# Kernel optimization log

Hardware: AMD Instinct MI355X
Metric: run time of the kernel (lower is better)

Reference implementation:

```python
import jax, jax.numpy as jnp
import numpy as np

CTX = 2048
N_EMBD = 1024
HEAD = 128

def setup_inputs() -> dict:
    key = jax.random.key(0)
    kx, kq, kk, kv = jax.random.split(key, 4)
    s = 1.0 / np.sqrt(N_EMBD)
    return {
        "x": jax.random.normal(kx, (4, CTX, N_EMBD), dtype=jnp.float32),
        "Wq": jax.random.normal(kq, (N_EMBD, HEAD), dtype=jnp.float32) * s,
        "Wk": jax.random.normal(kk, (N_EMBD, HEAD), dtype=jnp.float32) * s,
        "Wv": jax.random.normal(kv, (N_EMBD, HEAD), dtype=jnp.float32) * s,
    }

def reference(x, Wq, Wk, Wv):
    B, T, C = x.shape
    q = jnp.einsum('btc,ch->bth', x, Wq)
    k = jnp.einsum('btc,ch->bth', x, Wk)
    v = jnp.einsum('btc,ch->bth', x, Wv)
    scale = 1.0 / jnp.sqrt(jnp.asarray(k.shape[-1], dtype=x.dtype))
    wei = jnp.einsum('bth,bsh->bts', q, k) * scale  # [B,T,T]
    causal = jnp.tril(jnp.ones((T, T), dtype=bool))
    wei = jnp.where(causal, wei, jnp.asarray(-jnp.inf, dtype=wei.dtype))
    wei = jax.nn.softmax(wei, axis=-1)
    out = jnp.einsum('bts,bsh->bth', wei, v)
    return out
```

## Files before the change

### kernel.cpp

```cpp
#include <hip/hip_runtime.h>

#define BATCH 4
#define CTX   2048
#define EMB   1024
#define HEAD  128

typedef __attribute__((ext_vector_type(8))) short bf16x8;
typedef __attribute__((ext_vector_type(4))) float f32x4;
typedef const __attribute__((address_space(1))) unsigned int* gas_t;
typedef __attribute__((address_space(3))) unsigned int* las_t;

#define FINF (__builtin_inff())
__device__ inline float fexp2(float x) { return __builtin_amdgcn_exp2f(x); }

__device__ inline void cp16(const void* g, void* l) {
    __builtin_amdgcn_global_load_lds((gas_t)g, (las_t)l, 16, 0, 0);
}

__device__ inline unsigned short f2bf(float f) {
    union { float f; unsigned u; } v; v.f = f;
    unsigned r = v.u + 0x7fffu + ((v.u >> 16) & 1u);
    return (unsigned short)(r >> 16);
}
__device__ inline unsigned pk2(float a, float b) {
    return (unsigned)f2bf(a) | ((unsigned)f2bf(b) << 16);
}

__global__ __launch_bounds__(256)
void transpose_w_kernel(const float* __restrict__ Wq, const float* __restrict__ Wk,
                        const float* __restrict__ Wv, unsigned short* __restrict__ Wt) {
    const int k0 = blockIdx.x * 64;
    const int h0 = blockIdx.y * 64;
    const int w  = blockIdx.z;
    const float* W = (w == 0) ? Wq : (w == 1) ? Wk : Wv;
    __shared__ float Ts[64][65];
    const int tid = threadIdx.x;
    #pragma unroll
    for (int it = 0; it < 4; ++it) {
        const int kk = (tid >> 4) + it * 16;
        const int c4 = (tid & 15) * 4;
        const float4 f = *(const float4*)&W[(size_t)(k0 + kk) * HEAD + h0 + c4];
        Ts[kk][c4 + 0] = f.x; Ts[kk][c4 + 1] = f.y;
        Ts[kk][c4 + 2] = f.z; Ts[kk][c4 + 3] = f.w;
    }
    __syncthreads();
    const int hr  = tid >> 2;
    const int kc0 = (tid & 3) * 16;
    union { unsigned short s[16]; uint4 q[2]; } tmp;
    #pragma unroll
    for (int i = 0; i < 16; ++i) tmp.s[i] = f2bf(Ts[kc0 + i][hr]);
    unsigned short* dst = &Wt[(size_t)w * HEAD * EMB + (size_t)(h0 + hr) * EMB + k0 + kc0];
    ((uint4*)dst)[0] = tmp.q[0];
    ((uint4*)dst)[1] = tmp.q[1];
}

__global__ __launch_bounds__(128, 3)
void proj_kernel(const float* __restrict__ x, const unsigned short* __restrict__ Wt,
                 unsigned short* __restrict__ qb, unsigned short* __restrict__ kb,
                 unsigned short* __restrict__ vt) {
    __shared__ __align__(16) char smem[24576];
    char* Ab = smem;
    char* Bb = smem + 8192;

    const int wsel = blockIdx.y;
    const int tid  = threadIdx.x;
    const int wv   = tid >> 6;
    const int lane = tid & 63;
    const int p = lane >> 4, c = lane & 15;
    const int m0 = blockIdx.x * 32;
    const unsigned short* Wp = Wt + (size_t)wsel * HEAD * EMB;

    const int u7  = c & 7;
    const int u2c = (c ^ (c >> 2)) & 3;

    auto stage = [&](int bi, int ks) {
        #pragma unroll
        for (int i = 0; i < 2; ++i) {
            const int f = i * 128 + tid;
            const int r = f >> 3, s = f & 7, q = s ^ (r & 7);
            cp16(&x[(size_t)(m0 + r) * EMB + ks * 32 + q * 4],
                 Ab + bi * 4096 + i * 2048 + wv * 1024);
        }
        #pragma unroll
        for (int i = 0; i < 4; ++i) {
            const int f = i * 128 + tid;
            const int h = f >> 2, s = f & 3, q = s ^ ((h ^ (h >> 2)) & 3);
            cp16(&Wp[(size_t)h * EMB + ks * 32 + q * 8],
                 Bb + bi * 8192 + i * 2048 + wv * 1024);
        }
    };

    auto xfrag = [&](const char* Ac, int r) {
        const float4 a0 = *(const float4*)(Ac + r * 128 + (((2 * p)     ^ u7) * 16));
        const float4 a1 = *(const float4*)(Ac + r * 128 + (((2 * p + 1) ^ u7) * 16));
        union { unsigned u[4]; bf16x8 v; } xf;
        xf.u[0] = pk2(a0.x, a0.y); xf.u[1] = pk2(a0.z, a0.w);
        xf.u[2] = pk2(a1.x, a1.y); xf.u[3] = pk2(a1.z, a1.w);
        return xf.v;
    };

    if (wsel < 2) {
        f32x4 acc[8];
        #pragma unroll
        for (int i = 0; i < 8; ++i) acc[i] = (f32x4){0.f, 0.f, 0.f, 0.f};
        stage(0, 0);
        for (int ks = 0; ks < 32; ++ks) {
            const int cur = ks & 1;
            __syncthreads();
            if (ks + 1 < 32) stage(cur ^ 1, ks + 1);
            const bf16x8 xv = xfrag(Ab + cur * 4096, wv * 16 + c);
            const char* Bc = Bb + cur * 8192;
            #pragma unroll
            for (int nt = 0; nt < 8; ++nt) {
                const int h = nt * 16 + c;
                const bf16x8 wf = *(const bf16x8*)(Bc + h * 64 + ((p ^ u2c) * 16));
                acc[nt] = __builtin_amdgcn_mfma_f32_16x16x32_bf16(xv, wf, acc[nt], 0, 0, 0);
            }
        }
        unsigned short* outp = (wsel == 0) ? qb : kb;
        #pragma unroll
        for (int rr = 0; rr < 4; ++rr) {
            unsigned short* orow = outp + (size_t)(m0 + wv * 16 + p * 4 + rr) * HEAD + c;
            #pragma unroll
            for (int nt = 0; nt < 8; ++nt)
                orow[nt * 16] = f2bf(acc[nt][rr]);
        }
    } else {
        f32x4 acc[4][2];
        #pragma unroll
        for (int i = 0; i < 4; ++i)
            #pragma unroll
            for (int j = 0; j < 2; ++j) acc[i][j] = (f32x4){0.f, 0.f, 0.f, 0.f};
        stage(0, 0);
        for (int ks = 0; ks < 32; ++ks) {
            const int cur = ks & 1;
            __syncthreads();
            if (ks + 1 < 32) stage(cur ^ 1, ks + 1);
            const char* Ac = Ab + cur * 4096;
            const char* Bc = Bb + cur * 8192;
            bf16x8 xv[2];
            #pragma unroll
            for (int n2 = 0; n2 < 2; ++n2) xv[n2] = xfrag(Ac, n2 * 16 + c);
            #pragma unroll
            for (int mt = 0; mt < 4; ++mt) {
                const int h = wv * 64 + mt * 16 + c;
                const bf16x8 wf = *(const bf16x8*)(Bc + h * 64 + ((p ^ u2c) * 16));
                #pragma unroll
                for (int n2 = 0; n2 < 2; ++n2)
                    acc[mt][n2] = __builtin_amdgcn_mfma_f32_16x16x32_bf16(wf, xv[n2], acc[mt][n2], 0, 0, 0);
            }
        }
        const int bidx = m0 >> 11;
        const int tl   = m0 & (CTX - 1);
        unsigned short* vbp = vt + (size_t)bidx * HEAD * CTX;
        #pragma unroll
        for (int mt = 0; mt < 4; ++mt)
            #pragma unroll
            for (int rr = 0; rr < 4; ++rr) {
                const int h = wv * 64 + mt * 16 + p * 4 + rr;
                #pragma unroll
                for (int n2 = 0; n2 < 2; ++n2)
                    vbp[(size_t)h * CTX + tl + n2 * 16 + c] = f2bf(acc[mt][n2][rr]);
            }
    }
}

__global__ __launch_bounds__(64, 1)
void attn_kernel(const unsigned short* __restrict__ qb,
                 const unsigned short* __restrict__ kb,
                 const unsigned short* __restrict__ vt,
                 float* __restrict__ out) {
    __shared__ __align__(16) char smem[65536];
    char* Kb = smem;
    char* Vb = smem + 32768;

    const int bx   = blockIdx.x;
    const int b    = bx & 3;
    const int tile = 127 - (bx >> 2);
    const int lane = threadIdx.x;
    const int p = lane >> 4, c = lane & 15;
    const int t0 = tile * 16;
    const int qg = t0 + c;
    const int u7 = c & 7;

    const unsigned short* kbat = kb + (size_t)b * CTX * HEAD;
    const unsigned short* vbat = vt + (size_t)b * HEAD * CTX;

    bf16x8 qf[4];
    #pragma unroll
    for (int ks = 0; ks < 4; ++ks)
        qf[ks] = *(const bf16x8*)&qb[((size_t)b * CTX + t0 + c) * HEAD + ks * 32 + p * 8];

    f32x4 o[8];
    #pragma unroll
    for (int i = 0; i < 8; ++i) o[i] = (f32x4){0.f, 0.f, 0.f, 0.f};
    float m = -FINF, l = 0.f;

    const int  slA = 32 * (p & 1) + c;
    const int  slB = slA + 16;
    const bool thi = (p >> 1) != 0;
    const int  nsteps = (tile + 4) >> 2;
    const float scale2 = 0.08838834764831845f * 1.44269504088896340f;

    auto stage = [&](int bi, int js) {
        const unsigned short* kg = kbat + (size_t)(js * 64) * HEAD;
        #pragma unroll
        for (int i = 0; i < 16; ++i) {
            const int f = i * 64 + lane;
            const int r = f >> 4, s = f & 15, q = s ^ (r & 7);
            cp16(kg + (size_t)r * HEAD + q * 8, Kb + bi * 16384 + i * 1024);
        }
        #pragma unroll
        for (int i = 0; i < 16; ++i) {
            const int f = i * 64 + lane;
            const int r = f >> 3, s = f & 7, q = s ^ (r & 7);
            cp16(vbat + (size_t)r * CTX + js * 64 + q * 8, Vb + bi * 16384 + i * 1024);
        }
    };

    stage(0, 0);
    for (int js = 0; js < nsteps; ++js) {
        const int cur = js & 1;
        __builtin_amdgcn_s_waitcnt(0);

        bf16x8 kfr[4][4], vfr[2][8];
        #pragma unroll
        for (int nt = 0; nt < 4; ++nt) {
            const char* rp = Kb + cur * 16384 + (nt * 16 + c) * 256;
            #pragma unroll
            for (int ks = 0; ks < 4; ++ks)
                kfr[nt][ks] = *(const bf16x8*)(rp + (((ks * 4 + p) ^ u7) * 16));
        }
        #pragma unroll
        for (int mt = 0; mt < 8; ++mt) {
            const char* rp = Vb + cur * 16384 + (mt * 16 + c) * 128;
            #pragma unroll
            for (int ch = 0; ch < 2; ++ch)
                vfr[ch][mt] = *(const bf16x8*)(rp + (((ch * 4 + p) ^ u7) * 16));
        }

        if (js + 1 < nsteps) stage(cur ^ 1, js + 1);

        const int c0 = js * 64;
        f32x4 st[4];
        #pragma unroll
        for (int nt = 0; nt < 4; ++nt) st[nt] = (f32x4){0.f, 0.f, 0.f, 0.f};
        #pragma unroll
        for (int ks = 0; ks < 4; ++ks)
            #pragma unroll
            for (int nt = 0; nt < 4; ++nt)
                st[nt] = __builtin_amdgcn_mfma_f32_16x16x32_bf16(kfr[nt][ks], qf[ks], st[nt], 0, 0, 0);

        float s[4][4];
        float lm = -FINF;
        if (js == nsteps - 1) {
            #pragma unroll
            for (int nt = 0; nt < 4; ++nt)
                #pragma unroll
                for (int r = 0; r < 4; ++r) {
                    const int kv = c0 + nt * 16 + p * 4 + r;
                    float v = st[nt][r] * scale2;
                    v = (kv <= qg) ? v : -FINF;
                    s[nt][r] = v;
                    lm = fmaxf(lm, v);
                }
        } else {
            #pragma unroll
            for (int nt = 0; nt < 4; ++nt)
                #pragma unroll
                for (int r = 0; r < 4; ++r) {
                    const float v = st[nt][r] * scale2;
                    s[nt][r] = v;
                    lm = fmaxf(lm, v);
                }
        }
        lm = fmaxf(lm, __shfl_xor(lm, 16, 64));
        lm = fmaxf(lm, __shfl_xor(lm, 32, 64));
        const float m_new = fmaxf(m, lm);
        const float alpha = fexp2(m - m_new);
        float ls = 0.f;
        #pragma unroll
        for (int nt = 0; nt < 4; ++nt)
            #pragma unroll
            for (int r = 0; r < 4; ++r) {
                const float pv = fexp2(s[nt][r] - m_new);
                s[nt][r] = pv;
                ls += pv;
            }
        ls += __shfl_xor(ls, 16, 64);
        ls += __shfl_xor(ls, 32, 64);
        l = l * alpha + ls;
        m = m_new;
        #pragma unroll
        for (int i = 0; i < 8; ++i) {
            o[i][0] *= alpha; o[i][1] *= alpha;
            o[i][2] *= alpha; o[i][3] *= alpha;
        }
        #pragma unroll
        for (int ch = 0; ch < 2; ++ch) {
            const unsigned pa0 = pk2(s[2*ch][0],     s[2*ch][1]);
            const unsigned pb0 = pk2(s[2*ch][2],     s[2*ch][3]);
            const unsigned pa1 = pk2(s[2*ch + 1][0], s[2*ch + 1][1]);
            const unsigned pb1 = pk2(s[2*ch + 1][2], s[2*ch + 1][3]);
            const unsigned u0a = __shfl((int)pa0, slA, 64), u0b = __shfl((int)pa1, slA, 64);
            const unsigned u1a = __shfl((int)pb0, slA, 64), u1b = __shfl((int)pb1, slA, 64);
            const unsigned u2a = __shfl((int)pa0, slB, 64), u2b = __shfl((int)pa1, slB, 64);
            const unsigned u3a = __shfl((int)pb0, slB, 64), u3b = __shfl((int)pb1, slB, 64);
            union { unsigned u[4]; bf16x8 v; } pf;
            pf.u[0] = thi ? u0b : u0a;
            pf.u[1] = thi ? u1b : u1a;
            pf.u[2] = thi ? u2b : u2a;
            pf.u[3] = thi ? u3b : u3a;
            #pragma unroll
            for (int mt = 0; mt < 8; ++mt)
                o[mt] = __builtin_amdgcn_mfma_f32_16x16x32_bf16(vfr[ch][mt], pf.v, o[mt], 0, 0, 0);
        }
    }

    const float linv = 1.f / l;
    float* orow = out + ((size_t)b * CTX + t0 + c) * HEAD;
    #pragma unroll
    for (int mt = 0; mt < 8; ++mt) {
        float4 ov = make_float4(o[mt][0] * linv, o[mt][1] * linv,
                                o[mt][2] * linv, o[mt][3] * linv);
        *(float4*)&orow[mt * 16 + p * 4] = ov;
    }
}

extern "C" void kernel_launch(void* const* d_in, const int* in_sizes, int n_in,
                              void* d_out, int out_size, void* d_ws, size_t ws_size,
                              hipStream_t stream) {
    const float* x  = (const float*)d_in[0];
    const float* Wq = (const float*)d_in[1];
    const float* Wk = (const float*)d_in[2];
    const float* Wv = (const float*)d_in[3];
    float* out = (float*)d_out;

    unsigned short* Wt = (unsigned short*)d_ws;
    unsigned short* qb = Wt + (size_t)3 * HEAD * EMB;
    unsigned short* kb = qb + (size_t)BATCH * CTX * HEAD;
    unsigned short* vt = kb + (size_t)BATCH * CTX * HEAD;

    transpose_w_kernel<<<dim3(16, 2, 3), 256, 0, stream>>>(Wq, Wk, Wv, Wt);
    proj_kernel<<<dim3((BATCH * CTX) / 32, 3), 128, 0, stream>>>(x, Wt, qb, kb, vt);
    attn_kernel<<<BATCH * (CTX / 16), 64, 0, stream>>>(qb, kb, vt, out);
}
```

Measured before the change: 146.0 us.

## Split causal attention into KV chunks with partial outputs and a merge kernel

Replaces the single-wave-per-16-row attention kernel with a split-KV scheme. Each 256-thread block handles 64 query rows, and the KV range is cut into 512-key chunks so that long causal rows are spread over several blocks. Partial outputs go to workspace as bf16 along with the running max and sum, and a second kernel merges them with softmax rescaling. This aims to improve load balance and share each K/V tile across four waves, at the cost of an extra launch, workspace traffic and bf16 rounding of the partial outputs. It falls back to the old kernel if the workspace is too small.

```diff
diff --git a/kernel.cpp b/kernel.cpp
--- a/kernel.cpp
+++ b/kernel.cpp
@@ -24,6 +24,9 @@
 }
 __device__ inline unsigned pk2(float a, float b) {
     return (unsigned)f2bf(a) | ((unsigned)f2bf(b) << 16);
+}
+__device__ inline float bf2f(unsigned u16) {
+    union { unsigned u; float f; } v; v.u = u16 << 16; return v.f;
 }
 
 __global__ __launch_bounds__(256)
@@ -89,7 +92,6 @@
                  Bb + bi * 8192 + i * 2048 + wv * 1024);
         }
     };
-
     auto xfrag = [&](const char* Ac, int r) {
         const float4 a0 = *(const float4*)(Ac + r * 128 + (((2 * p)     ^ u7) * 16));
         const float4 a1 = *(const float4*)(Ac + r * 128 + (((2 * p + 1) ^ u7) * 16));
@@ -165,6 +167,236 @@
     }
 }
 
+__global__ __launch_bounds__(256, 2)
+void attn_split_kernel(const unsigned short* __restrict__ qb,
+                       const unsigned short* __restrict__ kb,
+                       const unsigned short* __restrict__ vt,
+                       unsigned short* __restrict__ pO,
+                       float* __restrict__ pM, float* __restrict__ pL) {
+    __shared__ __align__(16) char smem[65536];
+    char* Kb = smem;
+    char* Vb = smem + 32768;
+
+    const int g = blockIdx.x;
+    const int b = blockIdx.y;
+    int T, ch;
+    if (g < 8)       { T = g;                ch = 0; }
+    else if (g < 24) { T = 8  + ((g - 8) >> 1);  ch = (g - 8) & 1; }
+    else if (g < 48) { T = 16 + (g - 24) / 3;    ch = (g - 24) % 3; }
+    else             { T = 24 + ((g - 48) >> 2); ch = (g - 48) & 3; }
+    const int nch    = (T >> 3) + 1;
+    const int kstart = ch * 512;
+    const int kend   = min(kstart + 512, 64 * (T + 1));
+    const int nsteps = (kend - kstart) >> 6;
+    const bool lastchunk = (ch == nch - 1);
+
+    const int tid  = threadIdx.x;
+    const int wv   = tid >> 6;
+    const int lane = tid & 63;
+    const int p = lane >> 4, c = lane & 15;
+    const int t0 = T * 64;
+    const int qg = t0 + wv * 16 + c;
+    const int u7 = c & 7;
+
+    const unsigned short* kbat = kb + (size_t)b * CTX * HEAD;
+    const unsigned short* vbat = vt + (size_t)b * HEAD * CTX;
+
+    bf16x8 qf[4];
+    #pragma unroll
+    for (int ks = 0; ks < 4; ++ks)
+        qf[ks] = *(const bf16x8*)&qb[((size_t)b * CTX + t0 + wv * 16 + c) * HEAD + ks * 32 + p * 8];
+
+    f32x4 o[8];
+    #pragma unroll
+    for (int i = 0; i < 8; ++i) o[i] = (f32x4){0.f, 0.f, 0.f, 0.f};
+    float m = -FINF, l = 0.f;
+
+    const int  slA = 32 * (p & 1) + c;
+    const int  slB = slA + 16;
+    const bool thi = (p >> 1) != 0;
+    const float scale2 = 0.08838834764831845f * 1.44269504088896340f;
+
+    auto stage = [&](int bi, int js) {
+        const unsigned short* kg = kbat + (size_t)(kstart + js * 64) * HEAD;
+        #pragma unroll
+        for (int i = 0; i < 4; ++i) {
+            const int f = i * 256 + tid;
+            const int r = f >> 4, s = f & 15, q = s ^ (r & 7);
+            cp16(kg + (size_t)r * HEAD + q * 8, Kb + bi * 16384 + (f >> 6) * 1024);
+        }
+        const unsigned short* vg = vbat + kstart + js * 64;
+        #pragma unroll
+        for (int i = 0; i < 4; ++i) {
+            const int f = i * 256 + tid;
+            const int r = f >> 3, s = f & 7, q = s ^ (r & 7);
+            cp16(vg + (size_t)r * CTX + q * 8, Vb + bi * 16384 + (f >> 6) * 1024);
+        }
+    };
+
+    stage(0, 0);
+    for (int js = 0; js < nsteps; ++js) {
+        const int cur = js & 1;
+        __builtin_amdgcn_s_waitcnt(0);
+        __syncthreads();
+
+        bf16x8 kfr[4][4];
+        #pragma unroll
+        for (int nt = 0; nt < 4; ++nt) {
+            const char* rp = Kb + cur * 16384 + (nt * 16 + c) * 256;
+            #pragma unroll
+            for (int ks = 0; ks < 4; ++ks)
+                kfr[nt][ks] = *(const bf16x8*)(rp + (((ks * 4 + p) ^ u7) * 16));
+        }
+        if (js + 1 < nsteps) stage(cur ^ 1, js + 1);
+
+        f32x4 st[4];
+        #pragma unroll
+        for (int nt = 0; nt < 4; ++nt) st[nt] = (f32x4){0.f, 0.f, 0.f, 0.f};
+        #pragma unroll
+        for (int ks = 0; ks < 4; ++ks)
+            #pragma unroll
+            for (int nt = 0; nt < 4; ++nt)
+                st[nt] = __builtin_amdgcn_mfma_f32_16x16x32_bf16(kfr[nt][ks], qf[ks], st[nt], 0, 0, 0);
+
+        bf16x8 vfr[2][8];
+        #pragma unroll
+        for (int mt = 0; mt < 8; ++mt) {
+            const char* rp = Vb + cur * 16384 + (mt * 16 + c) * 128;
+            #pragma unroll
+            for (int ch2 = 0; ch2 < 2; ++ch2)
+                vfr[ch2][mt] = *(const bf16x8*)(rp + (((ch2 * 4 + p) ^ u7) * 16));
+        }
+
+        float s[4][4];
+        float lm = -FINF;
+        if (lastchunk && js == nsteps - 1) {
+            #pragma unroll
+            for (int nt = 0; nt < 4; ++nt)
+                #pragma unroll
+                for (int r = 0; r < 4; ++r) {
+                    const int kv = kstart + js * 64 + nt * 16 + p * 4 + r;
+                    float v = st[nt][r] * scale2;
+                    v = (kv <= qg) ? v : -FINF;
+                    s[nt][r] = v;
+                    lm = fmaxf(lm, v);
+                }
+        } else {
+            #pragma unroll
+            for (int nt = 0; nt < 4; ++nt)
+                #pragma unroll
+                for (int r = 0; r < 4; ++r) {
+                    const float v = st[nt][r] * scale2;
+                    s[nt][r] = v;
+                    lm = fmaxf(lm, v);
+                }
+        }
+        lm = fmaxf(lm, __shfl_xor(lm, 16, 64));
+        lm = fmaxf(lm, __shfl_xor(lm, 32, 64));
+        const float m_new = fmaxf(m, lm);
+        const float alpha = fexp2(m - m_new);
+        float ls = 0.f;
+        #pragma unroll
+        for (int nt = 0; nt < 4; ++nt)
+            #pragma unroll
+            for (int r = 0; r < 4; ++r) {
+                const float pv = fexp2(s[nt][r] - m_new);
+                s[nt][r] = pv;
+                ls += pv;
+            }
+        ls += __shfl_xor(ls, 16, 64);
+        ls += __shfl_xor(ls, 32, 64);
+        l = l * alpha + ls;
+        m = m_new;
+        #pragma unroll
+        for (int i = 0; i < 8; ++i) {
+            o[i][0] *= alpha; o[i][1] *= alpha;
+            o[i][2] *= alpha; o[i][3] *= alpha;
+        }
+        #pragma unroll
+        for (int ch2 = 0; ch2 < 2; ++ch2) {
+            const unsigned pa0 = pk2(s[2*ch2][0],     s[2*ch2][1]);
+            const unsigned pb0 = pk2(s[2*ch2][2],     s[2*ch2][3]);
+            const unsigned pa1 = pk2(s[2*ch2 + 1][0], s[2*ch2 + 1][1]);
+            const unsigned pb1 = pk2(s[2*ch2 + 1][2], s[2*ch2 + 1][3]);
+            const unsigned u0a = __shfl((int)pa0, slA, 64), u0b = __shfl((int)pa1, slA, 64);
+            const unsigned u1a = __shfl((int)pb0, slA, 64), u1b = __shfl((int)pb1, slA, 64);
+            const unsigned u2a = __shfl((int)pa0, slB, 64), u2b = __shfl((int)pa1, slB, 64);
+            const unsigned u3a = __shfl((int)pb0, slB, 64), u3b = __shfl((int)pb1, slB, 64);
+            union { unsigned u[4]; bf16x8 v; } pf;
+            pf.u[0] = thi ? u0b : u0a;
+            pf.u[1] = thi ? u1b : u1a;
+            pf.u[2] = thi ? u2b : u2a;
+            pf.u[3] = thi ? u3b : u3a;
+            #pragma unroll
+            for (int mt = 0; mt < 8; ++mt)
+                o[mt] = __builtin_amdgcn_mfma_f32_16x16x32_bf16(vfr[ch2][mt], pf.v, o[mt], 0, 0, 0);
+        }
+    }
+
+    const size_t pbase = (size_t)(b * 32 + T) * 4 + ch;
+    unsigned short* po = pO + pbase * (64 * 128) + (wv * 16 + c) * 128;
+    #pragma unroll
+    for (int mt = 0; mt < 8; ++mt) {
+        union { unsigned short sh[4]; uint2 u; } t;
+        #pragma unroll
+        for (int r = 0; r < 4; ++r) t.sh[r] = f2bf(o[mt][r]);
+        *(uint2*)&po[mt * 16 + p * 4] = t.u;
+    }
+    if (p == 0) {
+        pM[pbase * 64 + wv * 16 + c] = m;
+        pL[pbase * 64 + wv * 16 + c] = l;
+    }
+}
+
+__global__ __launch_bounds__(256)
+void attn_merge_kernel(const unsigned short* __restrict__ pO,
+                       const float* __restrict__ pM, const float* __restrict__ pL,
+                       float* __restrict__ out) {
+    const int T = blockIdx.x, b = blockIdx.y;
+    const int nch = (T >> 3) + 1;
+    const int tid = threadIdx.x;
+    const int r   = tid >> 2;
+    const int c0  = (tid & 3) * 32;
+    const size_t base = (size_t)(b * 32 + T) * 4;
+
+    float mv[4], lv[4];
+    float M = -FINF;
+    #pragma unroll
+    for (int i = 0; i < 4; ++i) {
+        if (i < nch) { mv[i] = pM[(base + i) * 64 + r]; lv[i] = pL[(base + i) * 64 + r]; }
+        else         { mv[i] = -FINF;                   lv[i] = 0.f; }
+        M = fmaxf(M, mv[i]);
+    }
+    float w[4], L = 0.f;
+    #pragma unroll
+    for (int i = 0; i < 4; ++i) { w[i] = fexp2(mv[i] - M); L += w[i] * lv[i]; }
+    const float inv = 1.f / L;
+
+    float acc[32];
+    #pragma unroll
+    for (int j = 0; j < 32; ++j) acc[j] = 0.f;
+    #pragma unroll
+    for (int i = 0; i < 4; ++i) {
+        if (i < nch) {
+            const unsigned* s32 = (const unsigned*)(pO + (base + i) * (64 * 128) + r * 128 + c0);
+            const float wi = w[i];
+            #pragma unroll
+            for (int jw = 0; jw < 16; ++jw) {
+                const unsigned u = s32[jw];
+                acc[2 * jw]     += wi * bf2f(u & 0xffffu);
+                acc[2 * jw + 1] += wi * bf2f(u >> 16);
+            }
+        }
+    }
+    float* orow = out + ((size_t)b * CTX + T * 64 + r) * HEAD + c0;
+    #pragma unroll
+    for (int j4 = 0; j4 < 8; ++j4) {
+        float4 ov = make_float4(acc[4*j4] * inv, acc[4*j4+1] * inv,
+                                acc[4*j4+2] * inv, acc[4*j4+3] * inv);
+        *(float4*)&orow[4 * j4] = ov;
+    }
+}
+
 __global__ __launch_bounds__(64, 1)
 void attn_kernel(const unsigned short* __restrict__ qb,
                  const unsigned short* __restrict__ kb,
@@ -173,7 +405,6 @@
     __shared__ __align__(16) char smem[65536];
     char* Kb = smem;
     char* Vb = smem + 32768;
-
     const int bx   = blockIdx.x;
     const int b    = bx & 3;
     const int tile = 127 - (bx >> 2);
@@ -182,26 +413,21 @@
     const int t0 = tile * 16;
     const int qg = t0 + c;
     const int u7 = c & 7;
-
     const unsigned short* kbat = kb + (size_t)b * CTX * HEAD;
     const unsigned short* vbat = vt + (size_t)b * HEAD * CTX;
-
     bf16x8 qf[4];
     #pragma unroll
     for (int ks = 0; ks < 4; ++ks)
         qf[ks] = *(const bf16x8*)&qb[((size_t)b * CTX + t0 + c) * HEAD + ks * 32 + p * 8];
-
     f32x4 o[8];
     #pragma unroll
     for (int i = 0; i < 8; ++i) o[i] = (f32x4){0.f, 0.f, 0.f, 0.f};
     float m = -FINF, l = 0.f;
-
     const int  slA = 32 * (p & 1) + c;
     const int  slB = slA + 16;
     const bool thi = (p >> 1) != 0;
     const int  nsteps = (tile + 4) >> 2;
     const float scale2 = 0.08838834764831845f * 1.44269504088896340f;
-
     auto stage = [&](int bi, int js) {
         const unsigned short* kg = kbat + (size_t)(js * 64) * HEAD;
         #pragma unroll
@@ -217,12 +443,10 @@
             cp16(vbat + (size_t)r * CTX + js * 64 + q * 8, Vb + bi * 16384 + i * 1024);
         }
     };
-
     stage(0, 0);
     for (int js = 0; js < nsteps; ++js) {
         const int cur = js & 1;
         __builtin_amdgcn_s_waitcnt(0);
-
         bf16x8 kfr[4][4], vfr[2][8];
         #pragma unroll
         for (int nt = 0; nt < 4; ++nt) {
@@ -238,9 +462,7 @@
             for (int ch = 0; ch < 2; ++ch)
                 vfr[ch][mt] = *(const bf16x8*)(rp + (((ch * 4 + p) ^ u7) * 16));
         }
-
         if (js + 1 < nsteps) stage(cur ^ 1, js + 1);
-
         const int c0 = js * 64;
         f32x4 st[4];
         #pragma unroll
@@ -250,7 +472,6 @@
             #pragma unroll
             for (int nt = 0; nt < 4; ++nt)
                 st[nt] = __builtin_amdgcn_mfma_f32_16x16x32_bf16(kfr[nt][ks], qf[ks], st[nt], 0, 0, 0);
-
         float s[4][4];
         float lm = -FINF;
         if (js == nsteps - 1) {
@@ -316,7 +537,6 @@
                 o[mt] = __builtin_amdgcn_mfma_f32_16x16x32_bf16(vfr[ch][mt], pf.v, o[mt], 0, 0, 0);
         }
     }
-
     const float linv = 1.f / l;
     float* orow = out + ((size_t)b * CTX + t0 + c) * HEAD;
     #pragma unroll
@@ -340,8 +560,18 @@
     unsigned short* qb = Wt + (size_t)3 * HEAD * EMB;
     unsigned short* kb = qb + (size_t)BATCH * CTX * HEAD;
     unsigned short* vt = kb + (size_t)BATCH * CTX * HEAD;
+    unsigned short* pO = vt + (size_t)BATCH * CTX * HEAD;
+    float* pM = (float*)(pO + (size_t)BATCH * 32 * 4 * 64 * 128);
+    float* pL = pM + (size_t)BATCH * 32 * 4 * 64;
+
+    const size_t need = (size_t)((char*)(pL + BATCH * 32 * 4 * 64) - (char*)d_ws);
 
     transpose_w_kernel<<<dim3(16, 2, 3), 256, 0, stream>>>(Wq, Wk, Wv, Wt);
     proj_kernel<<<dim3((BATCH * CTX) / 32, 3), 128, 0, stream>>>(x, Wt, qb, kb, vt);
-    attn_kernel<<<BATCH * (CTX / 16), 64, 0, stream>>>(qb, kb, vt, out);
-}
+    if (ws_size >= need) {
+        attn_split_kernel<<<dim3(80, 4), 256, 0, stream>>>(qb, kb, vt, pO, pM, pL);
+        attn_merge_kernel<<<dim3(32, 4), 256, 0, stream>>>(pO, pM, pL, out);
+    } else {
+        attn_kernel<<<BATCH * (CTX / 16), 64, 0, stream>>>(qb, kb, vt, out);
+    }
+}
```

New measurement: 126.0 us. 13.7% less time.
